# Performance work log

Hardware: AMD Instinct MI355X
Metric: run time of the kernel (lower is better)

The kernel has to match this reference:

```python
import jax, jax.numpy as jnp
import numpy as np
import math

DIM = 2048
N_HEADS = 16
HEAD_DIM = DIM // N_HEADS
BASE = 10000
B, S = 2, 2048


def rope_cache(seq_len, head_dim, base):
    theta = 1.0 / (base ** (jnp.arange(0, head_dim, 2, dtype=jnp.float32)[: head_dim // 2] / head_dim))
    idx_theta = jnp.arange(seq_len, dtype=jnp.float32)[:, None] * theta[None, :]  # [S, D/2]
    return jnp.cos(idx_theta), jnp.sin(idx_theta)


def apply_rope(x, cos, sin):
    # x: [B, S, H, D]; cos/sin: [S, D/2]; interleaved-pair rotation
    b, s, h, d = x.shape
    xr = x.astype(jnp.float32).reshape(b, s, h, d // 2, 2)
    c = cos[None, :, None, :]
    sn = sin[None, :, None, :]
    x0, x1 = xr[..., 0], xr[..., 1]
    out = jnp.stack([x0 * c - x1 * sn, x1 * c + x0 * sn], axis=-1)
    return out.reshape(b, s, h, d).astype(x.dtype)


def setup_inputs() -> dict:
    key = jax.random.key(0)
    k1, k2, k3, k4, k5 = jax.random.split(key, 5)
    x = jax.random.normal(k1, (B, S, DIM), dtype=jnp.float32)
    # causal mask: True = masked out (strict upper triangle)
    mask = jnp.triu(jnp.ones((S, S), dtype=bool), k=1)[None, None]  # [1,1,S,S]
    scale = 0.02
    wq = jax.random.normal(k2, (DIM, DIM), dtype=jnp.float32) * scale
    wk = jax.random.normal(k3, (DIM, DIM), dtype=jnp.float32) * scale
    wv = jax.random.normal(k4, (DIM, DIM), dtype=jnp.float32) * scale
    wo = jax.random.normal(k5, (DIM, DIM), dtype=jnp.float32) * scale
    return {"x": x, "mask": mask, "wq": wq, "wk": wk, "wv": wv, "wo": wo}


def reference(x, mask, wq, wk, wv, wo):
    b, s, _ = x.shape
    cos, sin = rope_cache(s, HEAD_DIM, BASE)
    q = (x @ wq.T).reshape(b, s, N_HEADS, HEAD_DIM)
    k = (x @ wk.T).reshape(b, s, N_HEADS, HEAD_DIM)
    v = (x @ wv.T).reshape(b, s, N_HEADS, HEAD_DIM)
    q = apply_rope(q, cos, sin)
    k = apply_rope(k, cos, sin)
    # [B, H, S, S]
    scores = jnp.einsum('bqhd,bkhd->bhqk', q, k) / math.sqrt(HEAD_DIM)
    scores = jnp.where(mask, -jnp.inf, scores)
    attn = jax.nn.softmax(scores.astype(jnp.float32), axis=-1).astype(q.dtype)
    out = jnp.einsum('bhqk,bkhd->bqhd', attn, v).reshape(b, s, DIM)
    return out @ wo.T
```

## Files before the change

### kernel.cpp

```cpp
#include <hip/hip_runtime.h>
#include <hip/hip_bf16.h>
#include <math.h>

#define DIM   2048
#define NH    16
#define HD    128
#define SEQ   2048
#define BATCH 2
#define QKVN  6144

typedef __attribute__((ext_vector_type(8))) short short8;
typedef __attribute__((ext_vector_type(4))) float f32x4;
typedef __attribute__((ext_vector_type(4))) unsigned int u32x4;
typedef __attribute__((ext_vector_type(4))) _Float16 half4;

static __device__ __forceinline__ unsigned short f2bf(float f) {
    __hip_bfloat16 h = __float2bfloat16(f);
    return *reinterpret_cast<unsigned short*>(&h);
}

static __device__ __forceinline__ void gload16(const void* g, void* l) {
    __builtin_amdgcn_global_load_lds(
        (const __attribute__((address_space(1))) void*)(g),
        (__attribute__((address_space(3))) void*)(l), 16, 0, 0);
}

__device__ __forceinline__ void storeC_helper(float* C, size_t idx, float v) { C[idx] = v; }
__device__ __forceinline__ void storeC_helper(__hip_bfloat16* C, size_t idx, float v) { C[idx] = __float2bfloat16(v); }

__global__ __launch_bounds__(256) void cast_all(const float* __restrict__ x,
                                                const float* __restrict__ wq,
                                                const float* __restrict__ wk,
                                                const float* __restrict__ wv,
                                                const float* __restrict__ wo,
                                                __hip_bfloat16* __restrict__ xb,
                                                __hip_bfloat16* __restrict__ wqkvb,
                                                __hip_bfloat16* __restrict__ wob) {
    const int VX = (BATCH * SEQ * DIM) / 4;
    const int VW = (DIM * DIM) / 4;
    int v = blockIdx.x * blockDim.x + threadIdx.x;
    const float* src; __hip_bfloat16* dst; int off;
    if (v < VX)               { src = x;  dst = xb;                            off = v; }
    else if (v < VX + VW)     { src = wq; dst = wqkvb;                         off = v - VX; }
    else if (v < VX + 2 * VW) { src = wk; dst = wqkvb + (size_t)DIM * DIM;     off = v - VX - VW; }
    else if (v < VX + 3 * VW) { src = wv; dst = wqkvb + 2ull * DIM * DIM;      off = v - VX - 2 * VW; }
    else                      { src = wo; dst = wob;                           off = v - VX - 3 * VW; }
    float4 f = *(const float4*)(src + (size_t)off * 4);
    union { unsigned short u[4]; uint2 d; } pk;
    pk.u[0] = f2bf(f.x); pk.u[1] = f2bf(f.y); pk.u[2] = f2bf(f.z); pk.u[3] = f2bf(f.w);
    *(uint2*)(dst + (size_t)off * 4) = pk.d;
}

template <int MODE, typename OutT>
__global__ __launch_bounds__(256) void gemm_bt(const __hip_bfloat16* __restrict__ A,
                                               const __hip_bfloat16* __restrict__ B,
                                               OutT* __restrict__ C,
                                               _Float16* __restrict__ vt,
                                               int M, int N, int K) {
    constexpr int BK = 64;
    __shared__ __align__(16) __hip_bfloat16 As[128 * BK];
    __shared__ __align__(16) __hip_bfloat16 Bs[128 * BK];
    int tid  = threadIdx.x;
    int lane = tid & 63;
    int wave = tid >> 6;
    int quad = lane >> 4;
    int l15  = lane & 15;
    int wr   = wave >> 1, wc = wave & 1;
    int m0 = blockIdx.y * 128;
    int n0 = blockIdx.x * 128;
    f32x4 acc[4][4] = {};

    for (int k0 = 0; k0 < K; k0 += BK) {
        __syncthreads();
#pragma unroll
        for (int c = 0; c < 4; c++) {
            int br = (wave * 4 + c) * 8;
            int r  = br + (lane >> 3);
            int cc = (lane & 7) ^ (r & 7);
            gload16(A + (size_t)(m0 + r) * K + k0 + cc * 8, As + br * 64);
            gload16(B + (size_t)(n0 + r) * K + k0 + cc * 8, Bs + br * 64);
        }
        __syncthreads();
#pragma unroll
        for (int kk = 0; kk < BK; kk += 32) {
            short8 af[4], bf4[4];
#pragma unroll
            for (int t = 0; t < 4; t++) {
                int Ra = wr * 64 + t * 16 + l15;
                int pa = ((kk >> 3) + quad) ^ (Ra & 7);
                af[t] = *(const short8*)(As + Ra * 64 + pa * 8);
                int Rb = wc * 64 + t * 16 + l15;
                int pb = ((kk >> 3) + quad) ^ (Rb & 7);
                bf4[t] = *(const short8*)(Bs + Rb * 64 + pb * 8);
            }
#pragma unroll
            for (int mt = 0; mt < 4; mt++)
#pragma unroll
                for (int nt = 0; nt < 4; nt++)
                    acc[mt][nt] = __builtin_amdgcn_mfma_f32_16x16x32_bf16(af[mt], bf4[nt], acc[mt][nt], 0, 0, 0);
        }
    }

    if (MODE == 1 && n0 >= 4096) {
        __syncthreads();
        _Float16* T = ((wave < 2) ? (_Float16*)As : (_Float16*)Bs) + (wave & 1) * 4096;
#pragma unroll
        for (int mt = 0; mt < 4; mt++)
#pragma unroll
            for (int nt = 0; nt < 4; nt++) {
                int dcol = nt * 16 + l15;
#pragma unroll
                for (int r = 0; r < 4; r++) {
                    int row = mt * 16 + quad * 4 + r;
                    int chunk = (row >> 3) ^ (dcol & 7);
                    T[dcol * 64 + chunk * 8 + (row & 7)] = (_Float16)acc[mt][nt][r];
                }
            }
        int h = (n0 - 4096) >> 7;
        int b = m0 >> 11;
        int sbase = (m0 & (SEQ - 1)) + wr * 64;
#pragma unroll
        for (int pass = 0; pass < 8; pass++) {
            int dl = pass * 8 + (lane >> 3);
            int sc = lane & 7;
            int chunk = sc ^ (dl & 7);
            u32x4 val = *(const u32x4*)(T + dl * 64 + chunk * 8);
            int d = wc * 64 + dl;
            *(u32x4*)(vt + ((size_t)((b * NH + h) * HD + d)) * SEQ + sbase + sc * 8) = val;
        }
        return;
    }

#pragma unroll
    for (int nt = 0; nt < 4; nt++) {
        int col = n0 + wc * 64 + nt * 16 + l15;
        float theta = 0.f;
        if (MODE == 1)
            theta = __expf(-((float)((col & 127) & ~1) * (1.0f / (float)HD)) * 9.210340371976184f);
#pragma unroll
        for (int mt = 0; mt < 4; mt++)
#pragma unroll
            for (int r = 0; r < 4; r++) {
                int row = m0 + wr * 64 + mt * 16 + quad * 4 + r;
                float val = acc[mt][nt][r];
                if (MODE == 1) {
                    float part = __shfl_xor(val, 1);
                    int s = row & (SEQ - 1);
                    float sn, cs;
                    __sincosf((float)s * theta, &sn, &cs);
                    val = (l15 & 1) ? val * cs + part * sn : val * cs - part * sn;
                }
                storeC_helper(C, (size_t)row * N + col, val);
            }
    }
}

__global__ __launch_bounds__(512, 2) void flash_kernel(const __hip_bfloat16* __restrict__ qkv,
                                                       const _Float16* __restrict__ vt,
                                                       __hip_bfloat16* __restrict__ attn) {
    __shared__ __align__(16) __hip_bfloat16 Ks[2][2][64 * 128];
    __shared__ __align__(16) _Float16 Vts[2][2][128 * 64];
    int tid  = threadIdx.x;
    int lane = tid & 63;
    int wave = tid >> 6;
    int grp  = wave >> 2;
    int wl   = wave & 3;
    int quad = lane >> 4;
    int l15  = lane & 15;
    int pairi = blockIdx.x;
    int bh = blockIdx.y;
    int b  = bh >> 4;
    int h  = bh & 15;
    size_t row0 = (size_t)b * SEQ;
    const _Float16* vbase = vt + (size_t)bh * HD * SEQ;
    const float scale = 0.08838834764831845f;
    const float NEG = -1e30f;

    auto stage = [&](int buf, int kt) {
#pragma unroll
        for (int c = 0; c < 4; c++) {
            int br = (wl * 4 + c) * 4;
            int r  = br + (lane >> 4);
            int cc = (lane & 15) ^ (r & 15);
            gload16(qkv + (row0 + kt * 64 + r) * (size_t)QKVN + DIM + h * HD + cc * 8,
                    &Ks[grp][buf][br * 128]);
        }
#pragma unroll
        for (int c = 0; c < 4; c++) {
            int br = (wl * 4 + c) * 8;
            int r  = br + (lane >> 3);
            int cc = (lane & 7) ^ ((r >> 1) & 7);
            gload16(vbase + (size_t)r * SEQ + kt * 64 + cc * 8, &Vts[grp][buf][br * 64]);
        }
    };

    for (int seg = 0; seg < 2; seg++) {
        int qt = seg ? (15 - pairi) : pairi;
        int half = qt + 1;
        int kbase = grp ? half : 0;

        short8 qf[2][4];
#pragma unroll
        for (int mt = 0; mt < 2; mt++) {
            int qrow = qt * 128 + wl * 32 + mt * 16 + l15;
            const __hip_bfloat16* qptr = qkv + (row0 + qrow) * (size_t)QKVN + h * HD + quad * 8;
#pragma unroll
            for (int c = 0; c < 4; c++) qf[mt][c] = *(const short8*)(qptr + c * 32);
        }
        f32x4 o[2][8] = {};
        float m_[2] = {NEG, NEG}, l_[2] = {0.f, 0.f};

        stage(0, kbase);

        for (int i = 0; i < half; i++) {
            __syncthreads();
            if (i + 1 < half) stage((i + 1) & 1, kbase + i + 1);
            int kt = kbase + i;
            const __hip_bfloat16* ks = Ks[grp][i & 1];
            const _Float16* vts = Vts[grp][i & 1];

            f32x4 s[2][4] = {};
#pragma unroll
            for (int ktile = 0; ktile < 4; ktile++) {
                int R = ktile * 16 + l15;
#pragma unroll
                for (int c = 0; c < 4; c++) {
                    int phys = (c * 4 + quad) ^ (R & 15);
                    short8 kf = *(const short8*)(ks + R * 128 + phys * 8);
                    s[0][ktile] = __builtin_amdgcn_mfma_f32_16x16x32_bf16(kf, qf[0][c], s[0][ktile], 0, 0, 0);
                    s[1][ktile] = __builtin_amdgcn_mfma_f32_16x16x32_bf16(kf, qf[1][c], s[1][ktile], 0, 0, 0);
                }
            }
            bool diag = (kt >= 2 * qt);
            float alpha[2];
#pragma unroll
            for (int mt = 0; mt < 2; mt++) {
                int q = qt * 128 + wl * 32 + mt * 16 + l15;
#pragma unroll
                for (int ktile = 0; ktile < 4; ktile++)
#pragma unroll
                    for (int r = 0; r < 4; r++) {
                        float v = s[mt][ktile][r] * scale;
                        if (diag) {
                            int key = kt * 64 + ktile * 16 + quad * 4 + r;
                            if (key > q) v = NEG;
                        }
                        s[mt][ktile][r] = v;
                    }
                float v = s[mt][0][0];
#pragma unroll
                for (int ktile = 0; ktile < 4; ktile++)
#pragma unroll
                    for (int r = 0; r < 4; r++) v = fmaxf(v, s[mt][ktile][r]);
                v = fmaxf(v, __shfl_xor(v, 16));
                v = fmaxf(v, __shfl_xor(v, 32));
                float mnew = fmaxf(m_[mt], v);
                alpha[mt] = __expf(m_[mt] - mnew);
                m_[mt] = mnew;
                float sum = 0.f;
#pragma unroll
                for (int ktile = 0; ktile < 4; ktile++)
#pragma unroll
                    for (int r = 0; r < 4; r++) {
                        float p = __expf(s[mt][ktile][r] - mnew);
                        s[mt][ktile][r] = p;
                        sum += p;
                    }
                sum += __shfl_xor(sum, 16);
                sum += __shfl_xor(sum, 32);
                l_[mt] = l_[mt] * alpha[mt] + sum;
#pragma unroll
                for (int dt = 0; dt < 8; dt++) o[mt][dt] *= alpha[mt];
            }
            half4 pk[2][4];
#pragma unroll
            for (int mt = 0; mt < 2; mt++)
#pragma unroll
                for (int kc = 0; kc < 4; kc++)
#pragma unroll
                    for (int r = 0; r < 4; r++) pk[mt][kc][r] = (_Float16)s[mt][kc][r];
#pragma unroll
            for (int kc = 0; kc < 4; kc++)
#pragma unroll
                for (int dt = 0; dt < 8; dt++) {
                    int d = dt * 16 + l15;
                    int c4 = ((kc * 4 + quad) ^ (d & 14));
                    half4 vf = *(const half4*)(vts + d * 64 + c4 * 4);
                    o[0][dt] = __builtin_amdgcn_mfma_f32_16x16x16f16(vf, pk[0][kc], o[0][dt], 0, 0, 0);
                    o[1][dt] = __builtin_amdgcn_mfma_f32_16x16x16f16(vf, pk[1][kc], o[1][dt], 0, 0, 0);
                }
        }

        __syncthreads();
        float* o1mb = (float*)&Ks[0][0][0];
        float* mlmb = (float*)&Vts[0][0][0];
        __hip_bfloat16* tb = (__hip_bfloat16*)((char*)&Vts[0][0][0] + 8192);
        if (grp == 1) {
            float* dst = o1mb + wl * 4096;
#pragma unroll
            for (int mt = 0; mt < 2; mt++)
#pragma unroll
                for (int dt = 0; dt < 8; dt++)
#pragma unroll
                    for (int r = 0; r < 4; r++)
                        dst[((mt * 8 + dt) * 4 + r) * 64 + lane] = o[mt][dt][r];
            float* ml = mlmb + (wl * 64 + lane) * 4;
            ml[0] = m_[0]; ml[1] = m_[1]; ml[2] = l_[0]; ml[3] = l_[1];
        }
        __syncthreads();
        if (grp == 0) {
            const float* src = o1mb + wl * 4096;
            const float* ml = mlmb + (wl * 64 + lane) * 4;
#pragma unroll
            for (int mt = 0; mt < 2; mt++) {
                float m1 = ml[mt], l1 = ml[2 + mt];
                float mm = fmaxf(m_[mt], m1);
                float a0 = __expf(m_[mt] - mm), a1 = __expf(m1 - mm);
                float linv = 1.0f / (l_[mt] * a0 + l1 * a1);
#pragma unroll
                for (int dt = 0; dt < 8; dt++)
#pragma unroll
                    for (int r = 0; r < 4; r++)
                        o[mt][dt][r] = (o[mt][dt][r] * a0 +
                                        src[((mt * 8 + dt) * 4 + r) * 64 + lane] * a1) * linv;
            }
            __hip_bfloat16* tw = tb + wl * 4096;
#pragma unroll
            for (int mt = 0; mt < 2; mt++)
#pragma unroll
                for (int dt = 0; dt < 8; dt++) {
                    int q32 = mt * 16 + l15;
                    int c4 = dt * 4 + quad;
                    int phys = c4 ^ ((q32 & 7) << 2);
                    union { unsigned short u[4]; uint2 dw; } pkb;
#pragma unroll
                    for (int r = 0; r < 4; r++) pkb.u[r] = f2bf(o[mt][dt][r]);
                    *(uint2*)(tw + q32 * 128 + phys * 4) = pkb.dw;
                }
#pragma unroll
            for (int pass = 0; pass < 8; pass++) {
                int q32 = pass * 4 + (lane >> 4);
                int p = l15;
                int phys = (p * 2) ^ ((q32 & 7) << 2);
                u32x4 val = *(const u32x4*)(tw + q32 * 128 + phys * 4);
                int qg = qt * 128 + wl * 32 + q32;
                *(u32x4*)(attn + (row0 + qg) * (size_t)DIM + h * HD + p * 8) = val;
            }
        }
        __syncthreads();
    }
}

extern "C" void kernel_launch(void* const* d_in, const int* in_sizes, int n_in,
                              void* d_out, int out_size, void* d_ws, size_t ws_size,
                              hipStream_t stream) {
    const float* x  = (const float*)d_in[0];
    const float* wq = (const float*)d_in[2];
    const float* wk = (const float*)d_in[3];
    const float* wv = (const float*)d_in[4];
    const float* wo = (const float*)d_in[5];
    float* out = (float*)d_out;

    char* ws = (char*)d_ws;
    __hip_bfloat16* xb    = (__hip_bfloat16*)(ws);
    __hip_bfloat16* attn  = (__hip_bfloat16*)(ws);
    __hip_bfloat16* wqkvb = (__hip_bfloat16*)(ws + 16777216ull);
    __hip_bfloat16* wob   = (__hip_bfloat16*)(ws + 41943040ull);
    __hip_bfloat16* qkv   = (__hip_bfloat16*)(ws + 50331648ull);
    _Float16*       vtg   = (_Float16*)(ws + 100663296ull);

    const int nv = (BATCH * SEQ * DIM + 4 * DIM * DIM) / 4;
    cast_all<<<nv / 256, 256, 0, stream>>>(x, wq, wk, wv, wo, xb, wqkvb, wob);

    gemm_bt<1, __hip_bfloat16><<<dim3(QKVN / 128, (BATCH * SEQ) / 128), 256, 0, stream>>>(
        xb, wqkvb, qkv, vtg, BATCH * SEQ, QKVN, DIM);

    flash_kernel<<<dim3(8, BATCH * NH), 512, 0, stream>>>(qkv, vtg, attn);

    gemm_bt<0, float><<<dim3(DIM / 128, (BATCH * SEQ) / 128), 256, 0, stream>>>(
        attn, wob, out, nullptr, BATCH * SEQ, DIM, DIM);
}
```

Baseline: 390.8 us.

## Use 256x256-tile pipelined GEMM kernel for QKV projection with fused RoPE

```diff
diff --git a/kernel.cpp b/kernel.cpp
--- a/kernel.cpp
+++ b/kernel.cpp
@@ -27,6 +27,11 @@
 
 __device__ __forceinline__ void storeC_helper(float* C, size_t idx, float v) { C[idx] = v; }
 __device__ __forceinline__ void storeC_helper(__hip_bfloat16* C, size_t idx, float v) { C[idx] = __float2bfloat16(v); }
+
+#define GFENCE()  asm volatile("" ::: "memory")
+#define GBAR()    do { GFENCE(); __builtin_amdgcn_s_barrier(); GFENCE(); } while (0)
+#define GWAITL0() do { asm volatile("s_waitcnt lgkmcnt(0)" ::: "memory"); __builtin_amdgcn_sched_barrier(0); } while (0)
+#define GWAITV(n) asm volatile("s_waitcnt vmcnt(" n ")" ::: "memory")
 
 __global__ __launch_bounds__(256) void cast_all(const float* __restrict__ x,
                                                 const float* __restrict__ wq,
@@ -51,6 +56,158 @@
     *(uint2*)(dst + (size_t)off * 4) = pk.d;
 }
 
+template <int MOFF>
+static __device__ __forceinline__ void mfma16(const short8* af, const short8* bf,
+                                              f32x4 (&acc)[8][4]) {
+    __builtin_amdgcn_s_setprio(1);
+#pragma unroll
+    for (int mt = 0; mt < 4; mt++)
+#pragma unroll
+        for (int nt = 0; nt < 4; nt++)
+            acc[MOFF + mt][nt] = __builtin_amdgcn_mfma_f32_16x16x32_bf16(
+                af[MOFF + mt], bf[nt], acc[MOFF + mt][nt], 0, 0, 0);
+    __builtin_amdgcn_s_setprio(0);
+}
+
+__global__ __launch_bounds__(512, 2) void gemm256_qkv(const __hip_bfloat16* __restrict__ A,
+                                                      const __hip_bfloat16* __restrict__ B,
+                                                      __hip_bfloat16* __restrict__ C,
+                                                      _Float16* __restrict__ vt) {
+    constexpr int K  = DIM;
+    constexpr int N  = QKVN;
+    constexpr int NT = K / 64;
+    constexpr int NI = NT / 2;
+    __shared__ __align__(16) __hip_bfloat16 As[2][256 * 64];
+    __shared__ __align__(16) __hip_bfloat16 Bs[2][256 * 64];
+
+    int tid  = threadIdx.x;
+    int lane = tid & 63;
+    int wave = tid >> 6;
+    int wm   = wave >> 2;
+    int wn   = wave & 3;
+    int quad = lane >> 4;
+    int l15  = lane & 15;
+    int m0   = blockIdx.y * 256;
+    int n0   = blockIdx.x * 256;
+
+    f32x4 acc[8][4] = {};
+
+    auto stage = [&](int tau, int h) {
+        const __hip_bfloat16* src;
+        __hip_bfloat16* dst;
+        if (h < 2) { src = A + (size_t)(m0 + h * 128) * K + tau * 64;
+                     dst = &As[tau & 1][h * 8192]; }
+        else       { src = B + (size_t)(n0 + (h - 2) * 128) * K + tau * 64;
+                     dst = &Bs[tau & 1][(h - 2) * 8192]; }
+#pragma unroll
+        for (int c = 0; c < 2; c++) {
+            int br = (wave * 2 + c) * 8;
+            int r  = br + (lane >> 3);
+            int cc = (lane & 7) ^ (r & 7);
+            gload16(src + (size_t)r * K + cc * 8, dst + br * 64);
+        }
+    };
+
+    int swz = l15 & 7;
+    const __hip_bfloat16* a00 = &As[0][(wm * 128 + l15) * 64 + ((quad    ) ^ swz) * 8];
+    const __hip_bfloat16* a01 = &As[0][(wm * 128 + l15) * 64 + ((4 + quad) ^ swz) * 8];
+    const __hip_bfloat16* b00 = &Bs[0][(wn * 64  + l15) * 64 + ((quad    ) ^ swz) * 8];
+    const __hip_bfloat16* b01 = &Bs[0][(wn * 64  + l15) * 64 + ((4 + quad) ^ swz) * 8];
+
+    short8 a0[8], a1[8], b0[4], b1[4];
+
+    stage(0, 0); stage(0, 1); stage(0, 2); stage(0, 3);
+    stage(1, 0); stage(1, 1); stage(1, 2);
+    GWAITV("6");
+    GBAR();
+
+#pragma unroll 1
+    for (int i = 0; i < NI; i++) {
+        const bool nl = (i < NI - 1);
+#pragma unroll
+        for (int mt = 0; mt < 8; mt++) a0[mt] = *(const short8*)(a00 + mt * 1024);
+#pragma unroll
+        for (int nt = 0; nt < 4; nt++) b0[nt] = *(const short8*)(b00 + nt * 1024);
+        stage(2 * i + 1, 3);
+        GBAR(); GWAITL0(); mfma16<0>(a0, b0, acc); GBAR();
+#pragma unroll
+        for (int mt = 0; mt < 8; mt++) a1[mt] = *(const short8*)(a01 + mt * 1024);
+#pragma unroll
+        for (int nt = 0; nt < 4; nt++) b1[nt] = *(const short8*)(b01 + nt * 1024);
+        GBAR(); GWAITL0(); mfma16<4>(a0, b0, acc); GBAR();
+        if (nl) stage(2 * i + 2, 0);
+        GBAR(); GWAITL0(); mfma16<0>(a1, b1, acc); GBAR();
+        if (nl) stage(2 * i + 2, 1);
+        GBAR(); GWAITL0(); mfma16<4>(a1, b1, acc);
+        if (nl) { GWAITV("4"); } else { GWAITV("0"); }
+        GBAR();
+#pragma unroll
+        for (int mt = 0; mt < 8; mt++) a0[mt] = *(const short8*)(a00 + 16384 + mt * 1024);
+#pragma unroll
+        for (int nt = 0; nt < 4; nt++) b0[nt] = *(const short8*)(b00 + 16384 + nt * 1024);
+        if (nl) stage(2 * i + 2, 2);
+        GBAR(); GWAITL0(); mfma16<0>(a0, b0, acc); GBAR();
+#pragma unroll
+        for (int mt = 0; mt < 8; mt++) a1[mt] = *(const short8*)(a01 + 16384 + mt * 1024);
+#pragma unroll
+        for (int nt = 0; nt < 4; nt++) b1[nt] = *(const short8*)(b01 + 16384 + nt * 1024);
+        if (nl) stage(2 * i + 2, 3);
+        GBAR(); GWAITL0(); mfma16<4>(a0, b0, acc); GBAR();
+        if (nl) { stage(2 * i + 3, 0); stage(2 * i + 3, 1); }
+        GBAR(); GWAITL0(); mfma16<0>(a1, b1, acc); GBAR();
+        if (nl) stage(2 * i + 3, 2);
+        GBAR(); GWAITL0(); mfma16<4>(a1, b1, acc);
+        if (nl) GWAITV("6");
+        GBAR();
+    }
+
+    int ncol0 = n0 + wn * 64;
+    if (ncol0 >= 4096) {
+        _Float16* T = ((wave < 4) ? (_Float16*)As : (_Float16*)Bs) + (wave & 3) * 8192;
+#pragma unroll
+        for (int mt = 0; mt < 8; mt++)
+#pragma unroll
+            for (int nt = 0; nt < 4; nt++) {
+                half4 hv;
+#pragma unroll
+                for (int r = 0; r < 4; r++) hv[r] = (_Float16)acc[mt][nt][r];
+                int chunk = mt * 2 + (quad >> 1);
+                int phys  = chunk ^ l15;
+                *(half4*)(T + (nt * 16 + l15) * 128 + phys * 8 + (quad & 1) * 4) = hv;
+            }
+        int h  = (ncol0 - 4096) >> 7;
+        int d0 = (ncol0 - 4096) & 127;
+        int b  = (m0 + wm * 128) >> 11;
+        int sb = (m0 + wm * 128) & (SEQ - 1);
+#pragma unroll
+        for (int pass = 0; pass < 16; pass++) {
+            int d = pass * 4 + quad;
+            int phys = l15 ^ (d & 15);
+            u32x4 val = *(const u32x4*)(T + d * 128 + phys * 8);
+            *(u32x4*)(vt + ((size_t)((b * NH + h) * HD + d0 + d)) * SEQ + sb + l15 * 8) = val;
+        }
+    } else {
+#pragma unroll
+        for (int nt = 0; nt < 4; nt++) {
+            int col = ncol0 + nt * 16 + l15;
+            float theta = __expf(-((float)((col & 127) & ~1) * (1.0f / (float)HD)) * 9.210340371976184f);
+#pragma unroll
+            for (int mt = 0; mt < 8; mt++)
+#pragma unroll
+                for (int r = 0; r < 4; r++) {
+                    int row = m0 + wm * 128 + mt * 16 + quad * 4 + r;
+                    float val = acc[mt][nt][r];
+                    float part = __shfl_xor(val, 1);
+                    int s = row & (SEQ - 1);
+                    float sn, cs;
+                    __sincosf((float)s * theta, &sn, &cs);
+                    val = (l15 & 1) ? val * cs + part * sn : val * cs - part * sn;
+                    C[(size_t)row * N + col] = __float2bfloat16(val);
+                }
+        }
+    }
+}
+
 template <int MODE, typename OutT>
 __global__ __launch_bounds__(256) void gemm_bt(const __hip_bfloat16* __restrict__ A,
                                                const __hip_bfloat16* __restrict__ B,
@@ -101,56 +258,15 @@
         }
     }
 
-    if (MODE == 1 && n0 >= 4096) {
-        __syncthreads();
-        _Float16* T = ((wave < 2) ? (_Float16*)As : (_Float16*)Bs) + (wave & 1) * 4096;
-#pragma unroll
-        for (int mt = 0; mt < 4; mt++)
-#pragma unroll
-            for (int nt = 0; nt < 4; nt++) {
-                int dcol = nt * 16 + l15;
-#pragma unroll
-                for (int r = 0; r < 4; r++) {
-                    int row = mt * 16 + quad * 4 + r;
-                    int chunk = (row >> 3) ^ (dcol & 7);
-                    T[dcol * 64 + chunk * 8 + (row & 7)] = (_Float16)acc[mt][nt][r];
-                }
-            }
-        int h = (n0 - 4096) >> 7;
-        int b = m0 >> 11;
-        int sbase = (m0 & (SEQ - 1)) + wr * 64;
-#pragma unroll
-        for (int pass = 0; pass < 8; pass++) {
-            int dl = pass * 8 + (lane >> 3);
-            int sc = lane & 7;
-            int chunk = sc ^ (dl & 7);
-            u32x4 val = *(const u32x4*)(T + dl * 64 + chunk * 8);
-            int d = wc * 64 + dl;
-            *(u32x4*)(vt + ((size_t)((b * NH + h) * HD + d)) * SEQ + sbase + sc * 8) = val;
-        }
-        return;
-    }
-
 #pragma unroll
     for (int nt = 0; nt < 4; nt++) {
         int col = n0 + wc * 64 + nt * 16 + l15;
-        float theta = 0.f;
-        if (MODE == 1)
-            theta = __expf(-((float)((col & 127) & ~1) * (1.0f / (float)HD)) * 9.210340371976184f);
 #pragma unroll
         for (int mt = 0; mt < 4; mt++)
 #pragma unroll
             for (int r = 0; r < 4; r++) {
                 int row = m0 + wr * 64 + mt * 16 + quad * 4 + r;
-                float val = acc[mt][nt][r];
-                if (MODE == 1) {
-                    float part = __shfl_xor(val, 1);
-                    int s = row & (SEQ - 1);
-                    float sn, cs;
-                    __sincosf((float)s * theta, &sn, &cs);
-                    val = (l15 & 1) ? val * cs + part * sn : val * cs - part * sn;
-                }
-                storeC_helper(C, (size_t)row * N + col, val);
+                storeC_helper(C, (size_t)row * N + col, acc[mt][nt][r]);
             }
     }
 }
@@ -372,8 +488,8 @@
     const int nv = (BATCH * SEQ * DIM + 4 * DIM * DIM) / 4;
     cast_all<<<nv / 256, 256, 0, stream>>>(x, wq, wk, wv, wo, xb, wqkvb, wob);
 
-    gemm_bt<1, __hip_bfloat16><<<dim3(QKVN / 128, (BATCH * SEQ) / 128), 256, 0, stream>>>(
-        xb, wqkvb, qkv, vtg, BATCH * SEQ, QKVN, DIM);
+    gemm256_qkv<<<dim3(QKVN / 256, (BATCH * SEQ) / 256), 512, 0, stream>>>(
+        xb, wqkvb, qkv, vtg);
 
     flash_kernel<<<dim3(8, BATCH * NH), 512, 0, stream>>>(qkv, vtg, attn);
 
```

Result: slower. 464.0 us (+18.7%).

## Replace paired-tile split-KV flash blocks with one query tile per 256-thread block

Applied to the files above, without the earlier changes.

```diff
diff --git a/kernel.cpp b/kernel.cpp
--- a/kernel.cpp
+++ b/kernel.cpp
@@ -155,19 +155,17 @@
     }
 }
 
-__global__ __launch_bounds__(512, 2) void flash_kernel(const __hip_bfloat16* __restrict__ qkv,
+__global__ __launch_bounds__(256, 2) void flash_kernel(const __hip_bfloat16* __restrict__ qkv,
                                                        const _Float16* __restrict__ vt,
                                                        __hip_bfloat16* __restrict__ attn) {
-    __shared__ __align__(16) __hip_bfloat16 Ks[2][2][64 * 128];
-    __shared__ __align__(16) _Float16 Vts[2][2][128 * 64];
+    __shared__ __align__(16) __hip_bfloat16 Ks[2][64 * 128];
+    __shared__ __align__(16) _Float16 Vts[2][128 * 64];
     int tid  = threadIdx.x;
     int lane = tid & 63;
-    int wave = tid >> 6;
-    int grp  = wave >> 2;
-    int wl   = wave & 3;
+    int wl   = tid >> 6;
     int quad = lane >> 4;
     int l15  = lane & 15;
-    int pairi = blockIdx.x;
+    int qt = 15 - blockIdx.x;
     int bh = blockIdx.y;
     int b  = bh >> 4;
     int h  = bh & 15;
@@ -183,171 +181,134 @@
             int r  = br + (lane >> 4);
             int cc = (lane & 15) ^ (r & 15);
             gload16(qkv + (row0 + kt * 64 + r) * (size_t)QKVN + DIM + h * HD + cc * 8,
-                    &Ks[grp][buf][br * 128]);
+                    &Ks[buf][br * 128]);
         }
 #pragma unroll
         for (int c = 0; c < 4; c++) {
             int br = (wl * 4 + c) * 8;
             int r  = br + (lane >> 3);
             int cc = (lane & 7) ^ ((r >> 1) & 7);
-            gload16(vbase + (size_t)r * SEQ + kt * 64 + cc * 8, &Vts[grp][buf][br * 64]);
+            gload16(vbase + (size_t)r * SEQ + kt * 64 + cc * 8, &Vts[buf][br * 64]);
         }
     };
 
-    for (int seg = 0; seg < 2; seg++) {
-        int qt = seg ? (15 - pairi) : pairi;
-        int half = qt + 1;
-        int kbase = grp ? half : 0;
-
-        short8 qf[2][4];
+    int ntiles = 2 * (qt + 1);
+
+    short8 qf[2][4];
+#pragma unroll
+    for (int mt = 0; mt < 2; mt++) {
+        int qrow = qt * 128 + wl * 32 + mt * 16 + l15;
+        const __hip_bfloat16* qptr = qkv + (row0 + qrow) * (size_t)QKVN + h * HD + quad * 8;
+#pragma unroll
+        for (int c = 0; c < 4; c++) qf[mt][c] = *(const short8*)(qptr + c * 32);
+    }
+    f32x4 o[2][8] = {};
+    float m_[2] = {NEG, NEG}, l_[2] = {0.f, 0.f};
+
+    stage(0, 0);
+
+    for (int i = 0; i < ntiles; i++) {
+        __syncthreads();
+        if (i + 1 < ntiles) stage((i + 1) & 1, i + 1);
+        const __hip_bfloat16* ks = Ks[i & 1];
+        const _Float16* vts = Vts[i & 1];
+
+        f32x4 s[2][4] = {};
+#pragma unroll
+        for (int ktile = 0; ktile < 4; ktile++) {
+            int R = ktile * 16 + l15;
+#pragma unroll
+            for (int c = 0; c < 4; c++) {
+                int phys = (c * 4 + quad) ^ (R & 15);
+                short8 kf = *(const short8*)(ks + R * 128 + phys * 8);
+                s[0][ktile] = __builtin_amdgcn_mfma_f32_16x16x32_bf16(kf, qf[0][c], s[0][ktile], 0, 0, 0);
+                s[1][ktile] = __builtin_amdgcn_mfma_f32_16x16x32_bf16(kf, qf[1][c], s[1][ktile], 0, 0, 0);
+            }
+        }
+        bool diag = (i >= 2 * qt);
+        float alpha[2];
 #pragma unroll
         for (int mt = 0; mt < 2; mt++) {
-            int qrow = qt * 128 + wl * 32 + mt * 16 + l15;
-            const __hip_bfloat16* qptr = qkv + (row0 + qrow) * (size_t)QKVN + h * HD + quad * 8;
-#pragma unroll
-            for (int c = 0; c < 4; c++) qf[mt][c] = *(const short8*)(qptr + c * 32);
-        }
-        f32x4 o[2][8] = {};
-        float m_[2] = {NEG, NEG}, l_[2] = {0.f, 0.f};
-
-        stage(0, kbase);
-
-        for (int i = 0; i < half; i++) {
-            __syncthreads();
-            if (i + 1 < half) stage((i + 1) & 1, kbase + i + 1);
-            int kt = kbase + i;
-            const __hip_bfloat16* ks = Ks[grp][i & 1];
-            const _Float16* vts = Vts[grp][i & 1];
-
-            f32x4 s[2][4] = {};
-#pragma unroll
-            for (int ktile = 0; ktile < 4; ktile++) {
-                int R = ktile * 16 + l15;
-#pragma unroll
-                for (int c = 0; c < 4; c++) {
-                    int phys = (c * 4 + quad) ^ (R & 15);
-                    short8 kf = *(const short8*)(ks + R * 128 + phys * 8);
-                    s[0][ktile] = __builtin_amdgcn_mfma_f32_16x16x32_bf16(kf, qf[0][c], s[0][ktile], 0, 0, 0);
-                    s[1][ktile] = __builtin_amdgcn_mfma_f32_16x16x32_bf16(kf, qf[1][c], s[1][ktile], 0, 0, 0);
+            int q = qt * 128 + wl * 32 + mt * 16 + l15;
+#pragma unroll
+            for (int ktile = 0; ktile < 4; ktile++)
+#pragma unroll
+                for (int r = 0; r < 4; r++) {
+                    float v = s[mt][ktile][r] * scale;
+                    if (diag) {
+                        int key = i * 64 + ktile * 16 + quad * 4 + r;
+                        if (key > q) v = NEG;
+                    }
+                    s[mt][ktile][r] = v;
                 }
-            }
-            bool diag = (kt >= 2 * qt);
-            float alpha[2];
-#pragma unroll
-            for (int mt = 0; mt < 2; mt++) {
-                int q = qt * 128 + wl * 32 + mt * 16 + l15;
-#pragma unroll
-                for (int ktile = 0; ktile < 4; ktile++)
-#pragma unroll
-                    for (int r = 0; r < 4; r++) {
-                        float v = s[mt][ktile][r] * scale;
-                        if (diag) {
-                            int key = kt * 64 + ktile * 16 + quad * 4 + r;
-                            if (key > q) v = NEG;
-                        }
-                        s[mt][ktile][r] = v;
-                    }
-                float v = s[mt][0][0];
-#pragma unroll
-                for (int ktile = 0; ktile < 4; ktile++)
-#pragma unroll
-                    for (int r = 0; r < 4; r++) v = fmaxf(v, s[mt][ktile][r]);
-                v = fmaxf(v, __shfl_xor(v, 16));
-                v = fmaxf(v, __shfl_xor(v, 32));
-                float mnew = fmaxf(m_[mt], v);
-                alpha[mt] = __expf(m_[mt] - mnew);
-                m_[mt] = mnew;
-                float sum = 0.f;
-#pragma unroll
-                for (int ktile = 0; ktile < 4; ktile++)
-#pragma unroll
-                    for (int r = 0; r < 4; r++) {
-                        float p = __expf(s[mt][ktile][r] - mnew);
-                        s[mt][ktile][r] = p;
-                        sum += p;
-                    }
-                sum += __shfl_xor(sum, 16);
-                sum += __shfl_xor(sum, 32);
-                l_[mt] = l_[mt] * alpha[mt] + sum;
-#pragma unroll
-                for (int dt = 0; dt < 8; dt++) o[mt][dt] *= alpha[mt];
-            }
-            half4 pk[2][4];
-#pragma unroll
-            for (int mt = 0; mt < 2; mt++)
-#pragma unroll
-                for (int kc = 0; kc < 4; kc++)
-#pragma unroll
-                    for (int r = 0; r < 4; r++) pk[mt][kc][r] = (_Float16)s[mt][kc][r];
+            float v = s[mt][0][0];
+#pragma unroll
+            for (int ktile = 0; ktile < 4; ktile++)
+#pragma unroll
+                for (int r = 0; r < 4; r++) v = fmaxf(v, s[mt][ktile][r]);
+            v = fmaxf(v, __shfl_xor(v, 16));
+            v = fmaxf(v, __shfl_xor(v, 32));
+            float mnew = fmaxf(m_[mt], v);
+            alpha[mt] = __expf(m_[mt] - mnew);
+            m_[mt] = mnew;
+            float sum = 0.f;
+#pragma unroll
+            for (int ktile = 0; ktile < 4; ktile++)
+#pragma unroll
+                for (int r = 0; r < 4; r++) {
+                    float p = __expf(s[mt][ktile][r] - mnew);
+                    s[mt][ktile][r] = p;
+                    sum += p;
+                }
+            sum += __shfl_xor(sum, 16);
+            sum += __shfl_xor(sum, 32);
+            l_[mt] = l_[mt] * alpha[mt] + sum;
+#pragma unroll
+            for (int dt = 0; dt < 8; dt++) o[mt][dt] *= alpha[mt];
+        }
+        half4 pk[2][4];
+#pragma unroll
+        for (int mt = 0; mt < 2; mt++)
 #pragma unroll
             for (int kc = 0; kc < 4; kc++)
 #pragma unroll
-                for (int dt = 0; dt < 8; dt++) {
-                    int d = dt * 16 + l15;
-                    int c4 = ((kc * 4 + quad) ^ (d & 14));
-                    half4 vf = *(const half4*)(vts + d * 64 + c4 * 4);
-                    o[0][dt] = __builtin_amdgcn_mfma_f32_16x16x16f16(vf, pk[0][kc], o[0][dt], 0, 0, 0);
-                    o[1][dt] = __builtin_amdgcn_mfma_f32_16x16x16f16(vf, pk[1][kc], o[1][dt], 0, 0, 0);
-                }
-        }
-
-        __syncthreads();
-        float* o1mb = (float*)&Ks[0][0][0];
-        float* mlmb = (float*)&Vts[0][0][0];
-        __hip_bfloat16* tb = (__hip_bfloat16*)((char*)&Vts[0][0][0] + 8192);
-        if (grp == 1) {
-            float* dst = o1mb + wl * 4096;
-#pragma unroll
-            for (int mt = 0; mt < 2; mt++)
-#pragma unroll
-                for (int dt = 0; dt < 8; dt++)
-#pragma unroll
-                    for (int r = 0; r < 4; r++)
-                        dst[((mt * 8 + dt) * 4 + r) * 64 + lane] = o[mt][dt][r];
-            float* ml = mlmb + (wl * 64 + lane) * 4;
-            ml[0] = m_[0]; ml[1] = m_[1]; ml[2] = l_[0]; ml[3] = l_[1];
-        }
-        __syncthreads();
-        if (grp == 0) {
-            const float* src = o1mb + wl * 4096;
-            const float* ml = mlmb + (wl * 64 + lane) * 4;
-#pragma unroll
-            for (int mt = 0; mt < 2; mt++) {
-                float m1 = ml[mt], l1 = ml[2 + mt];
-                float mm = fmaxf(m_[mt], m1);
-                float a0 = __expf(m_[mt] - mm), a1 = __expf(m1 - mm);
-                float linv = 1.0f / (l_[mt] * a0 + l1 * a1);
-#pragma unroll
-                for (int dt = 0; dt < 8; dt++)
-#pragma unroll
-                    for (int r = 0; r < 4; r++)
-                        o[mt][dt][r] = (o[mt][dt][r] * a0 +
-                                        src[((mt * 8 + dt) * 4 + r) * 64 + lane] * a1) * linv;
-            }
-            __hip_bfloat16* tw = tb + wl * 4096;
-#pragma unroll
-            for (int mt = 0; mt < 2; mt++)
-#pragma unroll
-                for (int dt = 0; dt < 8; dt++) {
-                    int q32 = mt * 16 + l15;
-                    int c4 = dt * 4 + quad;
-                    int phys = c4 ^ ((q32 & 7) << 2);
-                    union { unsigned short u[4]; uint2 dw; } pkb;
-#pragma unroll
-                    for (int r = 0; r < 4; r++) pkb.u[r] = f2bf(o[mt][dt][r]);
-                    *(uint2*)(tw + q32 * 128 + phys * 4) = pkb.dw;
-                }
-#pragma unroll
-            for (int pass = 0; pass < 8; pass++) {
-                int q32 = pass * 4 + (lane >> 4);
-                int p = l15;
-                int phys = (p * 2) ^ ((q32 & 7) << 2);
-                u32x4 val = *(const u32x4*)(tw + q32 * 128 + phys * 4);
-                int qg = qt * 128 + wl * 32 + q32;
-                *(u32x4*)(attn + (row0 + qg) * (size_t)DIM + h * HD + p * 8) = val;
-            }
-        }
-        __syncthreads();
+                for (int r = 0; r < 4; r++) pk[mt][kc][r] = (_Float16)s[mt][kc][r];
+#pragma unroll
+        for (int kc = 0; kc < 4; kc++)
+#pragma unroll
+            for (int dt = 0; dt < 8; dt++) {
+                int d = dt * 16 + l15;
+                int c4 = ((kc * 4 + quad) ^ (d & 14));
+                half4 vf = *(const half4*)(vts + d * 64 + c4 * 4);
+                o[0][dt] = __builtin_amdgcn_mfma_f32_16x16x16f16(vf, pk[0][kc], o[0][dt], 0, 0, 0);
+                o[1][dt] = __builtin_amdgcn_mfma_f32_16x16x16f16(vf, pk[1][kc], o[1][dt], 0, 0, 0);
+            }
+    }
+
+    __syncthreads();
+    __hip_bfloat16* tw = (__hip_bfloat16*)&Ks[0][0] + wl * 4096;
+#pragma unroll
+    for (int mt = 0; mt < 2; mt++) {
+        float linv = 1.0f / l_[mt];
+#pragma unroll
+        for (int dt = 0; dt < 8; dt++) {
+            int q32 = mt * 16 + l15;
+            int c4 = dt * 4 + quad;
+            int phys = c4 ^ ((q32 & 7) << 2);
+            union { unsigned short u[4]; uint2 dw; } pkb;
+#pragma unroll
+            for (int r = 0; r < 4; r++) pkb.u[r] = f2bf(o[mt][dt][r] * linv);
+            *(uint2*)(tw + q32 * 128 + phys * 4) = pkb.dw;
+        }
+    }
+#pragma unroll
+    for (int pass = 0; pass < 8; pass++) {
+        int q32 = pass * 4 + (lane >> 4);
+        int p = l15;
+        int phys = (p * 2) ^ ((q32 & 7) << 2);
+        u32x4 val = *(const u32x4*)(tw + q32 * 128 + phys * 4);
+        int qg = qt * 128 + wl * 32 + q32;
+        *(u32x4*)(attn + (row0 + qg) * (size_t)DIM + h * HD + p * 8) = val;
     }
 }
 
@@ -375,7 +336,7 @@
     gemm_bt<1, __hip_bfloat16><<<dim3(QKVN / 128, (BATCH * SEQ) / 128), 256, 0, stream>>>(
         xb, wqkvb, qkv, vtg, BATCH * SEQ, QKVN, DIM);
 
-    flash_kernel<<<dim3(8, BATCH * NH), 512, 0, stream>>>(qkv, vtg, attn);
+    flash_kernel<<<dim3(16, BATCH * NH), 256, 0, stream>>>(qkv, vtg, attn);
 
     gemm_bt<0, float><<<dim3(DIM / 128, (BATCH * SEQ) / 128), 256, 0, stream>>>(
         attn, wob, out, nullptr, BATCH * SEQ, DIM, DIM);
```

After: 417.2 us. 1.07x slower.
